# Performance work log

Measured on AMD Instinct MI355X. Metric: run time of the kernel, lower is better.

Reference implementation:

```python
import jax, jax.numpy as jnp
import numpy as np

N_NODES = 100000
N_EDGES = 640000
IN_CH, HID_CH, OUT_CH = 256, 128, 64


def setup_inputs() -> dict:
    key = jax.random.key(0)
    ks = jax.random.split(key, 6)
    x = jax.random.normal(ks[0], (N_NODES, IN_CH), dtype=jnp.float32)
    edge_index = jax.random.randint(ks[1], (2, N_EDGES), 0, N_NODES, dtype=jnp.int32)
    # Glorot-style init for GCNConv weights
    W1 = jax.random.normal(ks[2], (IN_CH, HID_CH), dtype=jnp.float32) * (1.0 / np.sqrt(IN_CH))
    W_mu = jax.random.normal(ks[3], (HID_CH, OUT_CH), dtype=jnp.float32) * (1.0 / np.sqrt(HID_CH))
    W_logvar = jax.random.normal(ks[4], (HID_CH, OUT_CH), dtype=jnp.float32) * (1.0 / np.sqrt(HID_CH))
    return {
        "x": x,
        "edge_index": edge_index,
        "W1": W1,
        "b1": jnp.zeros((HID_CH,), jnp.float32),
        "W_mu": W_mu,
        "b_mu": jnp.zeros((OUT_CH,), jnp.float32),
        "W_logvar": W_logvar,
        "b_logvar": jnp.zeros((OUT_CH,), jnp.float32),
    }


def reference(x, edge_index, W1, b1, W_mu, b_mu, W_logvar, b_logvar):
    N = x.shape[0]
    # PyG GCNConv default: add self-loops, symmetric normalization D^-1/2 A_hat D^-1/2
    loops = jnp.arange(N, dtype=edge_index.dtype)
    src = jnp.concatenate([edge_index[0], loops])  # [E+N]
    dst = jnp.concatenate([edge_index[1], loops])  # [E+N]
    deg = jax.ops.segment_sum(jnp.ones_like(src, dtype=x.dtype), dst, num_segments=N)
    dinv = jax.lax.rsqrt(deg)  # deg >= 1 due to self-loops
    norm = dinv[src] * dinv[dst]  # [E+N]

    def gcn_conv(h, W, b):
        h = h @ W                                   # [N, d_out]
        msg = h[src] * norm[:, None]                # gather + scale  [E+N, d_out]
        out = jax.ops.segment_sum(msg, dst, num_segments=N)  # scatter-add
        return out + b

    h = jax.nn.relu(gcn_conv(x, W1, b1))
    mu = gcn_conv(h, W_mu, b_mu)
    logvar = gcn_conv(h, W_logvar, b_logvar)
    return (mu, logvar)
```

## Files before the change

### kernel.cpp

```cpp
#include <hip/hip_runtime.h>
#include <hip/hip_bf16.h>

#define N_NODES 100000
#define E_EDGES 640000

typedef __attribute__((ext_vector_type(8))) short short8;
typedef __attribute__((ext_vector_type(4))) float float4v;

__device__ __forceinline__ float bf2f(unsigned int u16) {
    union { unsigned int i; float f; } c; c.i = u16 << 16; return c.f;
}
__device__ __forceinline__ unsigned short f2bf(float f) {
    union { float f; unsigned int i; } c; c.f = f;
    unsigned int x = c.i;
    unsigned int r = (x + 0x7fffu + ((x >> 16) & 1u)) >> 16;
    return (unsigned short)r;
}

#define WS_HIST    0
#define WS_CURSOR  524288
#define WS_OFFS    1048576
#define WS_DINV    1572864
#define WS_BSUMS   2097152
#define WS_ESRC    2621440
#define WS_EW      5242880
#define WS_WP1     7864320
#define WS_WP2     7995392
#define WS_H0      8388608
#define WS_H       34603008

__global__ __launch_bounds__(256) void k_init(int* __restrict__ hist, int* __restrict__ cursor) {
    int i = blockIdx.x * 256 + threadIdx.x;
    if (i < N_NODES) { hist[i] = 0; cursor[i] = 0; }
}

__global__ __launch_bounds__(256) void k_hist(const int* __restrict__ dst, int* __restrict__ hist) {
    int e = blockIdx.x * 256 + threadIdx.x;
    if (e < E_EDGES) atomicAdd(&hist[dst[e]], 1);
}

__global__ __launch_bounds__(256) void k_dinv(const int* __restrict__ hist, float* __restrict__ dinv) {
    int i = blockIdx.x * 256 + threadIdx.x;
    if (i < N_NODES) dinv[i] = rsqrtf((float)(hist[i] + 1));
}

__global__ __launch_bounds__(256) void k_scan1(const int* __restrict__ hist,
                                               int* __restrict__ offs,
                                               int* __restrict__ bsums) {
    __shared__ int sd[256];
    int t = threadIdx.x;
    int base = blockIdx.x * 1024 + t * 4;
    int v[4];
#pragma unroll
    for (int j = 0; j < 4; ++j) v[j] = (base + j < N_NODES) ? hist[base + j] : 0;
    int s = v[0] + v[1] + v[2] + v[3];
    sd[t] = s;
    __syncthreads();
    for (int d = 1; d < 256; d <<= 1) {
        int x = (t >= d) ? sd[t - d] : 0;
        __syncthreads();
        sd[t] += x;
        __syncthreads();
    }
    int excl = sd[t] - s;
    if (t == 255) bsums[blockIdx.x] = sd[255];
    int run = excl;
#pragma unroll
    for (int j = 0; j < 4; ++j) {
        if (base + j < N_NODES) offs[base + j] = run;
        run += v[j];
    }
}

__global__ __launch_bounds__(128) void k_scan2(int* __restrict__ bsums, int nb) {
    __shared__ int sd[128];
    int t = threadIdx.x;
    int v = (t < nb) ? bsums[t] : 0;
    sd[t] = v;
    __syncthreads();
    for (int d = 1; d < 128; d <<= 1) {
        int x = (t >= d) ? sd[t - d] : 0;
        __syncthreads();
        sd[t] += x;
        __syncthreads();
    }
    if (t < nb) bsums[t] = sd[t] - v;
}

__global__ __launch_bounds__(256) void k_scan3(int* __restrict__ offs, const int* __restrict__ bsums) {
    int i = blockIdx.x * 256 + threadIdx.x;
    if (i < N_NODES) offs[i] += bsums[i >> 10];
}

__global__ __launch_bounds__(256) void k_fill(const int* __restrict__ src, const int* __restrict__ dst,
                                              const int* __restrict__ offs, int* __restrict__ cursor,
                                              const float* __restrict__ dinv,
                                              int* __restrict__ esrc, float* __restrict__ ew) {
    int e = blockIdx.x * 256 + threadIdx.x;
    if (e < E_EDGES) {
        int s = src[e], d = dst[e];
        int p = offs[d] + atomicAdd(&cursor[d], 1);
        esrc[p] = s;
        ew[p] = dinv[s] * dinv[d];
    }
}

__global__ __launch_bounds__(256) void k_pack(const float* __restrict__ W1,
                                              const float* __restrict__ Wmu,
                                              const float* __restrict__ Wlv,
                                              unsigned short* __restrict__ Wp1,
                                              unsigned short* __restrict__ Wp2) {
    int i = blockIdx.x * 256 + threadIdx.x;
    if (i < 256 * 128) {
        int k = i >> 7, n = i & 127;
        Wp1[n * 256 + k] = f2bf(W1[i]);
    }
    if (i < 128 * 128) {
        int k = i >> 7, n = i & 127;
        float w = (n < 64) ? Wmu[k * 64 + n] : Wlv[k * 64 + (n - 64)];
        Wp2[n * 128 + k] = f2bf(w);
    }
}

template <int K, int AFP32, int MODE>
__global__ __launch_bounds__(256) void k_mgemm(const void* __restrict__ Ap,
                                               const unsigned short* __restrict__ Bpack,
                                               const float* __restrict__ bias0,
                                               const float* __restrict__ bias1,
                                               void* __restrict__ outp) {
    constexpr int LDT = 40;
    __shared__ unsigned short As[128 * LDT];
    __shared__ unsigned short Bs[128 * LDT];
    int tid = threadIdx.x;
    int row0 = blockIdx.x * 128;
    int wave = tid >> 6, lane = tid & 63;
    int c = lane & 15, q = lane >> 4;
    int wrow = (wave >> 1) * 64, wcol = (wave & 1) * 64;

    float4v acc[4][4];
#pragma unroll
    for (int i = 0; i < 4; ++i)
#pragma unroll
        for (int j = 0; j < 4; ++j) acc[i][j] = (float4v){0.f, 0.f, 0.f, 0.f};

    int srow = tid >> 1;
    int shalf = (tid & 1) * 16;
    const short8 zed = {0, 0, 0, 0, 0, 0, 0, 0};

    for (int k0 = 0; k0 < K; k0 += 32) {
        {
            const unsigned short* src = Bpack + (size_t)srow * K + k0 + shalf;
            short8 b0 = *(const short8*)(src);
            short8 b1 = *(const short8*)(src + 8);
            *(short8*)(&Bs[srow * LDT + shalf])     = b0;
            *(short8*)(&Bs[srow * LDT + shalf + 8]) = b1;
        }
        {
            int grow = row0 + srow;
            short8 a0 = zed, a1 = zed;
            if (AFP32) {
                if (grow < N_NODES) {
                    const float* src = (const float*)Ap + (size_t)grow * K + k0 + shalf;
                    float4v f0 = *(const float4v*)(src);
                    float4v f1 = *(const float4v*)(src + 4);
                    float4v f2 = *(const float4v*)(src + 8);
                    float4v f3 = *(const float4v*)(src + 12);
                    unsigned short t[16];
#pragma unroll
                    for (int j = 0; j < 4; ++j) t[j]      = f2bf(f0[j]);
#pragma unroll
                    for (int j = 0; j < 4; ++j) t[4 + j]  = f2bf(f1[j]);
#pragma unroll
                    for (int j = 0; j < 4; ++j) t[8 + j]  = f2bf(f2[j]);
#pragma unroll
                    for (int j = 0; j < 4; ++j) t[12 + j] = f2bf(f3[j]);
#pragma unroll
                    for (int j = 0; j < 8; ++j) a0[j] = (short)t[j];
#pragma unroll
                    for (int j = 0; j < 8; ++j) a1[j] = (short)t[8 + j];
                }
            } else {
                if (grow < N_NODES) {
                    const unsigned short* src = (const unsigned short*)Ap + (size_t)grow * K + k0 + shalf;
                    a0 = *(const short8*)(src);
                    a1 = *(const short8*)(src + 8);
                }
            }
            *(short8*)(&As[srow * LDT + shalf])     = a0;
            *(short8*)(&As[srow * LDT + shalf + 8]) = a1;
        }
        __syncthreads();

        short8 af[4], bfr[4];
#pragma unroll
        for (int mt = 0; mt < 4; ++mt)
            af[mt] = *(const short8*)(&As[(wrow + mt * 16 + c) * LDT + q * 8]);
#pragma unroll
        for (int nt = 0; nt < 4; ++nt)
            bfr[nt] = *(const short8*)(&Bs[(wcol + nt * 16 + c) * LDT + q * 8]);
#pragma unroll
        for (int mt = 0; mt < 4; ++mt)
#pragma unroll
            for (int nt = 0; nt < 4; ++nt)
                acc[mt][nt] = __builtin_amdgcn_mfma_f32_16x16x32_bf16(af[mt], bfr[nt], acc[mt][nt], 0, 0, 0);
        __syncthreads();
    }

#pragma unroll
    for (int mt = 0; mt < 4; ++mt) {
#pragma unroll
        for (int i = 0; i < 4; ++i) {
            int row = row0 + wrow + mt * 16 + q * 4 + i;
            if (row >= N_NODES) continue;
#pragma unroll
            for (int nt = 0; nt < 4; ++nt) {
                int cc = wcol + nt * 16 + c;
                float v = acc[mt][nt][i];
                if (MODE == 0) {
                    ((unsigned short*)outp)[(size_t)row * 128 + cc] = f2bf(v);
                } else {
                    float* o = (float*)outp;
                    if (cc < 64) o[(size_t)row * 64 + cc] = v + bias0[cc];
                    else o[(size_t)N_NODES * 64 + (size_t)row * 64 + (cc - 64)] = v + bias1[cc - 64];
                }
            }
        }
    }
}

template <bool RELU, bool BIAS>
__global__ __launch_bounds__(256) void k_agg(const unsigned int* __restrict__ in,
                                             unsigned int* __restrict__ out,
                                             const float* __restrict__ dinv,
                                             const int* __restrict__ esrc,
                                             const float* __restrict__ ew,
                                             const int* __restrict__ offs,
                                             const int* __restrict__ cnt,
                                             const float* __restrict__ bias) {
    int wid = (blockIdx.x * 256 + threadIdx.x) >> 6;
    if (wid >= N_NODES) return;
    int l = threadIdx.x & 63;
    float di = dinv[wid];
    unsigned int u = in[(size_t)wid * 64 + l];
    float vx = bf2f(u & 0xffffu), vy = bf2f(u >> 16);
    if (RELU) { vx = fmaxf(vx, 0.f); vy = fmaxf(vy, 0.f); }
    float sc = di * di;
    float ax = sc * vx, ay = sc * vy;
    if (BIAS) { ax += bias[2 * l]; ay += bias[2 * l + 1]; }
    int start = offs[wid];
    int n = cnt[wid];

    for (int base = 0; base < n; base += 64) {
        int m = min(n - base, 64);
        int sreg = 0; float wreg = 0.f;
        if (l < m) {
            sreg = esrc[start + base + l];
            wreg = ew[start + base + l];
        }
        int e = 0;
        for (; e + 4 <= m; e += 4) {
            int s0 = __shfl(sreg, e),     s1 = __shfl(sreg, e + 1);
            int s2 = __shfl(sreg, e + 2), s3 = __shfl(sreg, e + 3);
            float w0 = __shfl(wreg, e),     w1 = __shfl(wreg, e + 1);
            float w2 = __shfl(wreg, e + 2), w3 = __shfl(wreg, e + 3);
            unsigned int u0 = in[(size_t)s0 * 64 + l];
            unsigned int u1 = in[(size_t)s1 * 64 + l];
            unsigned int u2 = in[(size_t)s2 * 64 + l];
            unsigned int u3 = in[(size_t)s3 * 64 + l];
            float x0 = bf2f(u0 & 0xffffu), y0 = bf2f(u0 >> 16);
            float x1 = bf2f(u1 & 0xffffu), y1 = bf2f(u1 >> 16);
            float x2 = bf2f(u2 & 0xffffu), y2 = bf2f(u2 >> 16);
            float x3 = bf2f(u3 & 0xffffu), y3 = bf2f(u3 >> 16);
            if (RELU) {
                x0 = fmaxf(x0, 0.f); y0 = fmaxf(y0, 0.f);
                x1 = fmaxf(x1, 0.f); y1 = fmaxf(y1, 0.f);
                x2 = fmaxf(x2, 0.f); y2 = fmaxf(y2, 0.f);
                x3 = fmaxf(x3, 0.f); y3 = fmaxf(y3, 0.f);
            }
            ax += w0 * x0; ay += w0 * y0;
            ax += w1 * x1; ay += w1 * y1;
            ax += w2 * x2; ay += w2 * y2;
            ax += w3 * x3; ay += w3 * y3;
        }
        for (; e < m; ++e) {
            int s0 = __shfl(sreg, e);
            float w0 = __shfl(wreg, e);
            unsigned int u0 = in[(size_t)s0 * 64 + l];
            float x0 = bf2f(u0 & 0xffffu), y0 = bf2f(u0 >> 16);
            if (RELU) { x0 = fmaxf(x0, 0.f); y0 = fmaxf(y0, 0.f); }
            ax += w0 * x0; ay += w0 * y0;
        }
    }
    out[(size_t)wid * 64 + l] = (unsigned int)f2bf(ax) | ((unsigned int)f2bf(ay) << 16);
}

extern "C" void kernel_launch(void* const* d_in, const int* in_sizes, int n_in,
                              void* d_out, int out_size, void* d_ws, size_t ws_size,
                              hipStream_t stream) {
    const float* x    = (const float*)d_in[0];
    const int*   ei   = (const int*)d_in[1];
    const float* W1   = (const float*)d_in[2];
    const float* b1   = (const float*)d_in[3];
    const float* Wmu  = (const float*)d_in[4];
    const float* bmu  = (const float*)d_in[5];
    const float* Wlv  = (const float*)d_in[6];
    const float* blv  = (const float*)d_in[7];
    float* outp = (float*)d_out;

    const int* src = ei;
    const int* dst = ei + E_EDGES;

    char* ws = (char*)d_ws;
    int*            hist   = (int*)(ws + WS_HIST);
    int*            cursor = (int*)(ws + WS_CURSOR);
    int*            offs   = (int*)(ws + WS_OFFS);
    float*          dinv   = (float*)(ws + WS_DINV);
    int*            bsums  = (int*)(ws + WS_BSUMS);
    int*            esrc   = (int*)(ws + WS_ESRC);
    float*          ew     = (float*)(ws + WS_EW);
    unsigned short* Wp1    = (unsigned short*)(ws + WS_WP1);
    unsigned short* Wp2    = (unsigned short*)(ws + WS_WP2);
    unsigned short* h0     = (unsigned short*)(ws + WS_H0);
    unsigned short* h      = (unsigned short*)(ws + WS_H);

    const int NB_N = (N_NODES + 255) / 256;
    const int NB_E = (E_EDGES + 255) / 256;
    const int NB_S = (N_NODES + 1023) / 1024;
    const int NB_G = (N_NODES + 127) / 128;

    k_init<<<NB_N, 256, 0, stream>>>(hist, cursor);
    k_hist<<<NB_E, 256, 0, stream>>>(dst, hist);
    k_dinv<<<NB_N, 256, 0, stream>>>(hist, dinv);
    k_scan1<<<NB_S, 256, 0, stream>>>(hist, offs, bsums);
    k_scan2<<<1, 128, 0, stream>>>(bsums, NB_S);
    k_scan3<<<NB_N, 256, 0, stream>>>(offs, bsums);
    k_fill<<<NB_E, 256, 0, stream>>>(src, dst, offs, cursor, dinv, esrc, ew);
    k_pack<<<128, 256, 0, stream>>>(W1, Wmu, Wlv, Wp1, Wp2);

    k_mgemm<256, 1, 0><<<NB_G, 256, 0, stream>>>(x, Wp1, nullptr, nullptr, h0);
    k_agg<false, true><<<(N_NODES * 64 + 255) / 256, 256, 0, stream>>>(
        (const unsigned int*)h0, (unsigned int*)h, dinv, esrc, ew, offs, hist, b1);

    k_agg<true, false><<<(N_NODES * 64 + 255) / 256, 256, 0, stream>>>(
        (const unsigned int*)h, (unsigned int*)h0, dinv, esrc, ew, offs, hist, nullptr);
    k_mgemm<128, 0, 1><<<NB_G, 256, 0, stream>>>(h0, Wp2, bmu, blv, outp);
}
```

Measured before the change: 368.2 us.

## Fuse second aggregation into output GEMM, pack edge data, async-load GEMM A tiles

After: 431.6 us. 17.2% more time.

```diff
diff --git a/kernel.cpp b/kernel.cpp
--- a/kernel.cpp
+++ b/kernel.cpp
@@ -17,42 +17,40 @@
     return (unsigned short)r;
 }
 
+#define ASYNC16(g, l)                                                          \
+    __builtin_amdgcn_global_load_lds(                                          \
+        (const __attribute__((address_space(1))) void*)(g),                    \
+        (__attribute__((address_space(3))) void*)(l), 16, 0, 0)
+
 #define WS_HIST    0
 #define WS_CURSOR  524288
 #define WS_OFFS    1048576
 #define WS_DINV    1572864
 #define WS_BSUMS   2097152
-#define WS_ESRC    2621440
-#define WS_EW      5242880
+#define WS_EIDX    2621440
 #define WS_WP1     7864320
-#define WS_WP2     7995392
-#define WS_H0      8388608
-#define WS_H       34603008
-
-__global__ __launch_bounds__(256) void k_init(int* __restrict__ hist, int* __restrict__ cursor) {
-    int i = blockIdx.x * 256 + threadIdx.x;
-    if (i < N_NODES) { hist[i] = 0; cursor[i] = 0; }
-}
+#define WS_WP2     7929856
+#define WS_H0      7962624
+#define WS_H       33562624
 
 __global__ __launch_bounds__(256) void k_hist(const int* __restrict__ dst, int* __restrict__ hist) {
     int e = blockIdx.x * 256 + threadIdx.x;
     if (e < E_EDGES) atomicAdd(&hist[dst[e]], 1);
 }
 
-__global__ __launch_bounds__(256) void k_dinv(const int* __restrict__ hist, float* __restrict__ dinv) {
-    int i = blockIdx.x * 256 + threadIdx.x;
-    if (i < N_NODES) dinv[i] = rsqrtf((float)(hist[i] + 1));
-}
-
 __global__ __launch_bounds__(256) void k_scan1(const int* __restrict__ hist,
                                                int* __restrict__ offs,
-                                               int* __restrict__ bsums) {
+                                               int* __restrict__ bsums,
+                                               float* __restrict__ dinv) {
     __shared__ int sd[256];
     int t = threadIdx.x;
     int base = blockIdx.x * 1024 + t * 4;
     int v[4];
 #pragma unroll
     for (int j = 0; j < 4; ++j) v[j] = (base + j < N_NODES) ? hist[base + j] : 0;
+#pragma unroll
+    for (int j = 0; j < 4; ++j)
+        if (base + j < N_NODES) dinv[base + j] = rsqrtf((float)(v[j] + 1));
     int s = v[0] + v[1] + v[2] + v[3];
     sd[t] = s;
     __syncthreads();
@@ -95,13 +93,15 @@
 __global__ __launch_bounds__(256) void k_fill(const int* __restrict__ src, const int* __restrict__ dst,
                                               const int* __restrict__ offs, int* __restrict__ cursor,
                                               const float* __restrict__ dinv,
-                                              int* __restrict__ esrc, float* __restrict__ ew) {
+                                              int2* __restrict__ eidx) {
     int e = blockIdx.x * 256 + threadIdx.x;
     if (e < E_EDGES) {
         int s = src[e], d = dst[e];
         int p = offs[d] + atomicAdd(&cursor[d], 1);
-        esrc[p] = s;
-        ew[p] = dinv[s] * dinv[d];
+        int2 v;
+        v.x = s;
+        v.y = __float_as_int(dinv[s] * dinv[d]);
+        eidx[p] = v;
     }
 }
 
@@ -122,15 +122,11 @@
     }
 }
 
-template <int K, int AFP32, int MODE>
-__global__ __launch_bounds__(256) void k_mgemm(const void* __restrict__ Ap,
-                                               const unsigned short* __restrict__ Bpack,
-                                               const float* __restrict__ bias0,
-                                               const float* __restrict__ bias1,
-                                               void* __restrict__ outp) {
-    constexpr int LDT = 40;
-    __shared__ unsigned short As[128 * LDT];
-    __shared__ unsigned short Bs[128 * LDT];
+__global__ __launch_bounds__(256) void k_mgemm1(const float* __restrict__ A,
+                                                const unsigned short* __restrict__ Bpack,
+                                                unsigned short* __restrict__ out) {
+    __shared__ float As[128 * 32];
+    __shared__ unsigned short Bs[128 * 40];
     int tid = threadIdx.x;
     int row0 = blockIdx.x * 128;
     int wave = tid >> 6, lane = tid & 63;
@@ -145,59 +141,41 @@
 
     int srow = tid >> 1;
     int shalf = (tid & 1) * 16;
-    const short8 zed = {0, 0, 0, 0, 0, 0, 0, 0};
-
-    for (int k0 = 0; k0 < K; k0 += 32) {
-        {
-            const unsigned short* src = Bpack + (size_t)srow * K + k0 + shalf;
-            short8 b0 = *(const short8*)(src);
-            short8 b1 = *(const short8*)(src + 8);
-            *(short8*)(&Bs[srow * LDT + shalf])     = b0;
-            *(short8*)(&Bs[srow * LDT + shalf + 8]) = b1;
-        }
-        {
-            int grow = row0 + srow;
-            short8 a0 = zed, a1 = zed;
-            if (AFP32) {
-                if (grow < N_NODES) {
-                    const float* src = (const float*)Ap + (size_t)grow * K + k0 + shalf;
-                    float4v f0 = *(const float4v*)(src);
-                    float4v f1 = *(const float4v*)(src + 4);
-                    float4v f2 = *(const float4v*)(src + 8);
-                    float4v f3 = *(const float4v*)(src + 12);
-                    unsigned short t[16];
-#pragma unroll
-                    for (int j = 0; j < 4; ++j) t[j]      = f2bf(f0[j]);
-#pragma unroll
-                    for (int j = 0; j < 4; ++j) t[4 + j]  = f2bf(f1[j]);
-#pragma unroll
-                    for (int j = 0; j < 4; ++j) t[8 + j]  = f2bf(f2[j]);
-#pragma unroll
-                    for (int j = 0; j < 4; ++j) t[12 + j] = f2bf(f3[j]);
-#pragma unroll
-                    for (int j = 0; j < 8; ++j) a0[j] = (short)t[j];
-#pragma unroll
-                    for (int j = 0; j < 8; ++j) a1[j] = (short)t[8 + j];
-                }
-            } else {
-                if (grow < N_NODES) {
-                    const unsigned short* src = (const unsigned short*)Ap + (size_t)grow * K + k0 + shalf;
-                    a0 = *(const short8*)(src);
-                    a1 = *(const short8*)(src + 8);
-                }
-            }
-            *(short8*)(&As[srow * LDT + shalf])     = a0;
-            *(short8*)(&As[srow * LDT + shalf + 8]) = a1;
-        }
+
+    for (int k0 = 0; k0 < 256; k0 += 32) {
+        const unsigned short* bsrc = Bpack + (size_t)srow * 256 + k0 + shalf;
+        short8 b0 = *(const short8*)(bsrc);
+        short8 b1 = *(const short8*)(bsrc + 8);
+#pragma unroll
+        for (int t = 0; t < 4; ++t) {
+            int S = (t * 4 + wave) * 64 + lane;
+            int row = S >> 3, j = S & 7;
+            int kq = j ^ (row & 7);
+            const float* g = A + (size_t)(row0 + row) * 256 + k0 + kq * 4;
+            float* ldst = As + (t * 4 + wave) * 256;
+            if (row0 + row < N_NODES) ASYNC16(g, ldst);
+        }
+        *(short8*)(&Bs[srow * 40 + shalf])     = b0;
+        *(short8*)(&Bs[srow * 40 + shalf + 8]) = b1;
         __syncthreads();
 
         short8 af[4], bfr[4];
 #pragma unroll
-        for (int mt = 0; mt < 4; ++mt)
-            af[mt] = *(const short8*)(&As[(wrow + mt * 16 + c) * LDT + q * 8]);
+        for (int mt = 0; mt < 4; ++mt) {
+            int r = wrow + mt * 16 + c;
+            int j0 = (q * 2) ^ (r & 7);
+            float4v fa = *(const float4v*)(&As[r * 32 + j0 * 4]);
+            float4v fb = *(const float4v*)(&As[r * 32 + (j0 ^ 1) * 4]);
+            short8 s;
+#pragma unroll
+            for (int jj = 0; jj < 4; ++jj) s[jj]     = (short)f2bf(fa[jj]);
+#pragma unroll
+            for (int jj = 0; jj < 4; ++jj) s[4 + jj] = (short)f2bf(fb[jj]);
+            af[mt] = s;
+        }
 #pragma unroll
         for (int nt = 0; nt < 4; ++nt)
-            bfr[nt] = *(const short8*)(&Bs[(wcol + nt * 16 + c) * LDT + q * 8]);
+            bfr[nt] = *(const short8*)(&Bs[(wcol + nt * 16 + c) * 40 + q * 8]);
 #pragma unroll
         for (int mt = 0; mt < 4; ++mt)
 #pragma unroll
@@ -215,38 +193,27 @@
 #pragma unroll
             for (int nt = 0; nt < 4; ++nt) {
                 int cc = wcol + nt * 16 + c;
-                float v = acc[mt][nt][i];
-                if (MODE == 0) {
-                    ((unsigned short*)outp)[(size_t)row * 128 + cc] = f2bf(v);
-                } else {
-                    float* o = (float*)outp;
-                    if (cc < 64) o[(size_t)row * 64 + cc] = v + bias0[cc];
-                    else o[(size_t)N_NODES * 64 + (size_t)row * 64 + (cc - 64)] = v + bias1[cc - 64];
-                }
+                out[(size_t)row * 128 + cc] = f2bf(acc[mt][nt][i]);
             }
         }
     }
 }
 
-template <bool RELU, bool BIAS>
-__global__ __launch_bounds__(256) void k_agg(const unsigned int* __restrict__ in,
-                                             unsigned int* __restrict__ out,
-                                             const float* __restrict__ dinv,
-                                             const int* __restrict__ esrc,
-                                             const float* __restrict__ ew,
-                                             const int* __restrict__ offs,
-                                             const int* __restrict__ cnt,
-                                             const float* __restrict__ bias) {
+__global__ __launch_bounds__(256) void k_agg1(const unsigned int* __restrict__ in,
+                                              unsigned int* __restrict__ out,
+                                              const float* __restrict__ dinv,
+                                              const int2* __restrict__ eidx,
+                                              const int* __restrict__ offs,
+                                              const int* __restrict__ cnt,
+                                              const float* __restrict__ bias) {
     int wid = (blockIdx.x * 256 + threadIdx.x) >> 6;
     if (wid >= N_NODES) return;
     int l = threadIdx.x & 63;
     float di = dinv[wid];
     unsigned int u = in[(size_t)wid * 64 + l];
-    float vx = bf2f(u & 0xffffu), vy = bf2f(u >> 16);
-    if (RELU) { vx = fmaxf(vx, 0.f); vy = fmaxf(vy, 0.f); }
     float sc = di * di;
-    float ax = sc * vx, ay = sc * vy;
-    if (BIAS) { ax += bias[2 * l]; ay += bias[2 * l + 1]; }
+    float ax = sc * bf2f(u & 0xffffu) + bias[2 * l];
+    float ay = sc * bf2f(u >> 16) + bias[2 * l + 1];
     int start = offs[wid];
     int n = cnt[wid];
 
@@ -254,8 +221,9 @@
         int m = min(n - base, 64);
         int sreg = 0; float wreg = 0.f;
         if (l < m) {
-            sreg = esrc[start + base + l];
-            wreg = ew[start + base + l];
+            int2 ev = eidx[start + base + l];
+            sreg = ev.x;
+            wreg = __int_as_float(ev.y);
         }
         int e = 0;
         for (; e + 4 <= m; e += 4) {
@@ -267,31 +235,130 @@
             unsigned int u1 = in[(size_t)s1 * 64 + l];
             unsigned int u2 = in[(size_t)s2 * 64 + l];
             unsigned int u3 = in[(size_t)s3 * 64 + l];
-            float x0 = bf2f(u0 & 0xffffu), y0 = bf2f(u0 >> 16);
-            float x1 = bf2f(u1 & 0xffffu), y1 = bf2f(u1 >> 16);
-            float x2 = bf2f(u2 & 0xffffu), y2 = bf2f(u2 >> 16);
-            float x3 = bf2f(u3 & 0xffffu), y3 = bf2f(u3 >> 16);
-            if (RELU) {
-                x0 = fmaxf(x0, 0.f); y0 = fmaxf(y0, 0.f);
-                x1 = fmaxf(x1, 0.f); y1 = fmaxf(y1, 0.f);
-                x2 = fmaxf(x2, 0.f); y2 = fmaxf(y2, 0.f);
-                x3 = fmaxf(x3, 0.f); y3 = fmaxf(y3, 0.f);
-            }
-            ax += w0 * x0; ay += w0 * y0;
-            ax += w1 * x1; ay += w1 * y1;
-            ax += w2 * x2; ay += w2 * y2;
-            ax += w3 * x3; ay += w3 * y3;
+            ax += w0 * bf2f(u0 & 0xffffu); ay += w0 * bf2f(u0 >> 16);
+            ax += w1 * bf2f(u1 & 0xffffu); ay += w1 * bf2f(u1 >> 16);
+            ax += w2 * bf2f(u2 & 0xffffu); ay += w2 * bf2f(u2 >> 16);
+            ax += w3 * bf2f(u3 & 0xffffu); ay += w3 * bf2f(u3 >> 16);
         }
         for (; e < m; ++e) {
             int s0 = __shfl(sreg, e);
             float w0 = __shfl(wreg, e);
             unsigned int u0 = in[(size_t)s0 * 64 + l];
-            float x0 = bf2f(u0 & 0xffffu), y0 = bf2f(u0 >> 16);
-            if (RELU) { x0 = fmaxf(x0, 0.f); y0 = fmaxf(y0, 0.f); }
-            ax += w0 * x0; ay += w0 * y0;
-        }
-    }
+            ax += w0 * bf2f(u0 & 0xffffu); ay += w0 * bf2f(u0 >> 16);
+        }
+    }
+    ax = fmaxf(ax, 0.f); ay = fmaxf(ay, 0.f);
     out[(size_t)wid * 64 + l] = (unsigned int)f2bf(ax) | ((unsigned int)f2bf(ay) << 16);
+}
+
+__global__ __launch_bounds__(256) void k_aggemm(const unsigned int* __restrict__ hr,
+                                                const int2* __restrict__ eidx,
+                                                const int* __restrict__ offs,
+                                                const int* __restrict__ cnt,
+                                                const float* __restrict__ dinv,
+                                                const unsigned short* __restrict__ Wp2,
+                                                const float* __restrict__ bias0,
+                                                const float* __restrict__ bias1,
+                                                float* __restrict__ out) {
+    __shared__ unsigned short As[128 * 136];
+    __shared__ unsigned short Bs[128 * 40];
+    int tid = threadIdx.x, wave = tid >> 6, lane = tid & 63;
+    int row0 = blockIdx.x * 128;
+
+    for (int nn = 0; nn < 32; ++nn) {
+        int r = wave * 32 + nn;
+        int node = row0 + r;
+        float ax = 0.f, ay = 0.f;
+        if (node < N_NODES) {
+            float di = dinv[node];
+            unsigned int u = hr[(size_t)node * 64 + lane];
+            float sc = di * di;
+            ax = sc * bf2f(u & 0xffffu);
+            ay = sc * bf2f(u >> 16);
+            int start = offs[node];
+            int n = cnt[node];
+            for (int base = 0; base < n; base += 64) {
+                int m = min(n - base, 64);
+                int sreg = 0; float wreg = 0.f;
+                if (lane < m) {
+                    int2 ev = eidx[start + base + lane];
+                    sreg = ev.x;
+                    wreg = __int_as_float(ev.y);
+                }
+                int e = 0;
+                for (; e + 4 <= m; e += 4) {
+                    int s0 = __shfl(sreg, e),     s1 = __shfl(sreg, e + 1);
+                    int s2 = __shfl(sreg, e + 2), s3 = __shfl(sreg, e + 3);
+                    float w0 = __shfl(wreg, e),     w1 = __shfl(wreg, e + 1);
+                    float w2 = __shfl(wreg, e + 2), w3 = __shfl(wreg, e + 3);
+                    unsigned int u0 = hr[(size_t)s0 * 64 + lane];
+                    unsigned int u1 = hr[(size_t)s1 * 64 + lane];
+                    unsigned int u2 = hr[(size_t)s2 * 64 + lane];
+                    unsigned int u3 = hr[(size_t)s3 * 64 + lane];
+                    ax += w0 * bf2f(u0 & 0xffffu); ay += w0 * bf2f(u0 >> 16);
+                    ax += w1 * bf2f(u1 & 0xffffu); ay += w1 * bf2f(u1 >> 16);
+                    ax += w2 * bf2f(u2 & 0xffffu); ay += w2 * bf2f(u2 >> 16);
+                    ax += w3 * bf2f(u3 & 0xffffu); ay += w3 * bf2f(u3 >> 16);
+                }
+                for (; e < m; ++e) {
+                    int s0 = __shfl(sreg, e);
+                    float w0 = __shfl(wreg, e);
+                    unsigned int u0 = hr[(size_t)s0 * 64 + lane];
+                    ax += w0 * bf2f(u0 & 0xffffu); ay += w0 * bf2f(u0 >> 16);
+                }
+            }
+        }
+        *(unsigned int*)(&As[r * 136 + 2 * lane]) =
+            (unsigned int)f2bf(ax) | ((unsigned int)f2bf(ay) << 16);
+    }
+    __syncthreads();
+
+    int c = lane & 15, q = lane >> 4;
+    int wrow = (wave >> 1) * 64, wcol = (wave & 1) * 64;
+    float4v acc[4][4];
+#pragma unroll
+    for (int i = 0; i < 4; ++i)
+#pragma unroll
+        for (int j = 0; j < 4; ++j) acc[i][j] = (float4v){0.f, 0.f, 0.f, 0.f};
+    int srow = tid >> 1, shalf = (tid & 1) * 16;
+
+    for (int k0 = 0; k0 < 128; k0 += 32) {
+        const unsigned short* bsrc = Wp2 + (size_t)srow * 128 + k0 + shalf;
+        short8 b0 = *(const short8*)(bsrc);
+        short8 b1 = *(const short8*)(bsrc + 8);
+        *(short8*)(&Bs[srow * 40 + shalf])     = b0;
+        *(short8*)(&Bs[srow * 40 + shalf + 8]) = b1;
+        __syncthreads();
+        short8 af[4], bfr[4];
+#pragma unroll
+        for (int mt = 0; mt < 4; ++mt)
+            af[mt] = *(const short8*)(&As[(wrow + mt * 16 + c) * 136 + k0 + q * 8]);
+#pragma unroll
+        for (int nt = 0; nt < 4; ++nt)
+            bfr[nt] = *(const short8*)(&Bs[(wcol + nt * 16 + c) * 40 + q * 8]);
+#pragma unroll
+        for (int mt = 0; mt < 4; ++mt)
+#pragma unroll
+            for (int nt = 0; nt < 4; ++nt)
+                acc[mt][nt] = __builtin_amdgcn_mfma_f32_16x16x32_bf16(af[mt], bfr[nt], acc[mt][nt], 0, 0, 0);
+        __syncthreads();
+    }
+
+#pragma unroll
+    for (int mt = 0; mt < 4; ++mt) {
+#pragma unroll
+        for (int i = 0; i < 4; ++i) {
+            int row = row0 + wrow + mt * 16 + q * 4 + i;
+            if (row >= N_NODES) continue;
+#pragma unroll
+            for (int nt = 0; nt < 4; ++nt) {
+                int cc = wcol + nt * 16 + c;
+                float v = acc[mt][nt][i];
+                if (cc < 64) out[(size_t)row * 64 + cc] = v + bias0[cc];
+                else out[(size_t)N_NODES * 64 + (size_t)row * 64 + (cc - 64)] = v + bias1[cc - 64];
+            }
+        }
+    }
 }
 
 extern "C" void kernel_launch(void* const* d_in, const int* in_sizes, int n_in,
@@ -316,8 +383,7 @@
     int*            offs   = (int*)(ws + WS_OFFS);
     float*          dinv   = (float*)(ws + WS_DINV);
     int*            bsums  = (int*)(ws + WS_BSUMS);
-    int*            esrc   = (int*)(ws + WS_ESRC);
-    float*          ew     = (float*)(ws + WS_EW);
+    int2*           eidx   = (int2*)(ws + WS_EIDX);
     unsigned short* Wp1    = (unsigned short*)(ws + WS_WP1);
     unsigned short* Wp2    = (unsigned short*)(ws + WS_WP2);
     unsigned short* h0     = (unsigned short*)(ws + WS_H0);
@@ -328,20 +394,18 @@
     const int NB_S = (N_NODES + 1023) / 1024;
     const int NB_G = (N_NODES + 127) / 128;
 
-    k_init<<<NB_N, 256, 0, stream>>>(hist, cursor);
+    hipMemsetAsync(ws + WS_HIST, 0, 1048576, stream);
     k_hist<<<NB_E, 256, 0, stream>>>(dst, hist);
-    k_dinv<<<NB_N, 256, 0, stream>>>(hist, dinv);
-    k_scan1<<<NB_S, 256, 0, stream>>>(hist, offs, bsums);
+    k_scan1<<<NB_S, 256, 0, stream>>>(hist, offs, bsums, dinv);
     k_scan2<<<1, 128, 0, stream>>>(bsums, NB_S);
     k_scan3<<<NB_N, 256, 0, stream>>>(offs, bsums);
-    k_fill<<<NB_E, 256, 0, stream>>>(src, dst, offs, cursor, dinv, esrc, ew);
+    k_fill<<<NB_E, 256, 0, stream>>>(src, dst, offs, cursor, dinv, eidx);
     k_pack<<<128, 256, 0, stream>>>(W1, Wmu, Wlv, Wp1, Wp2);
 
-    k_mgemm<256, 1, 0><<<NB_G, 256, 0, stream>>>(x, Wp1, nullptr, nullptr, h0);
-    k_agg<false, true><<<(N_NODES * 64 + 255) / 256, 256, 0, stream>>>(
-        (const unsigned int*)h0, (unsigned int*)h, dinv, esrc, ew, offs, hist, b1);
-
-    k_agg<true, false><<<(N_NODES * 64 + 255) / 256, 256, 0, stream>>>(
-        (const unsigned int*)h, (unsigned int*)h0, dinv, esrc, ew, offs, hist, nullptr);
-    k_mgemm<128, 0, 1><<<NB_G, 256, 0, stream>>>(h0, Wp2, bmu, blv, outp);
-}
+    k_mgemm1<<<NB_G, 256, 0, stream>>>(x, Wp1, h0);
+    k_agg1<<<(N_NODES * 64 + 255) / 256, 256, 0, stream>>>(
+        (const unsigned int*)h0, (unsigned int*)h, dinv, eidx, offs, hist, b1);
+
+    k_aggemm<<<NB_G, 256, 0, stream>>>(
+        (const unsigned int*)h, eidx, offs, hist, dinv, Wp2, bmu, blv, outp);
+}
```
